# Performance work log

Measured on AMD Instinct MI355X. Metric: run time of the kernel, lower is better.

The kernel has to match this reference:

```python
import jax, jax.numpy as jnp
import numpy as np

N = 50000      # nodes
E = 600000     # message-passing edges (avg degree 12)
P = 500000     # candidate pairs
DH = 128       # d_h
NRBF = 16      # n_rbf
NL = 3         # n_layers
RBF_MAX = 1.5  # coords in [0,1]^2 -> max dist sqrt(2) ~ 1.414


def _mlp2(x, W1, b1, W2, b2):
    # mlp([a, b, c]) = Linear(a,b) -> ReLU -> Linear(b,c); dropout=0.0 is a no-op
    return jnp.dot(jax.nn.relu(jnp.dot(x, W1) + b1), W2) + b2


def _rbf(r):
    # Gaussian radial basis expansion of edge distances, NRBF centers on [0, RBF_MAX]
    centers = jnp.linspace(0.0, RBF_MAX, NRBF, dtype=r.dtype)
    width = centers[1] - centers[0]
    return jnp.exp(-jnp.square((r[:, None] - centers) / width))


def setup_inputs() -> dict:
    key = jax.random.key(0)
    ks = jax.random.split(key, 24)

    def lin(k, fan_in, fan_out):
        return jax.random.normal(k, (fan_in, fan_out), dtype=jnp.float32) / np.sqrt(fan_in)

    def lin_stack(k, n, fan_in, fan_out):
        return jax.random.normal(k, (n, fan_in, fan_out), dtype=jnp.float32) / np.sqrt(fan_in)

    inp = {}
    inp["coords01"] = jax.random.uniform(ks[0], (N, 2), dtype=jnp.float32)
    inp["msg_edge_index"] = jax.random.randint(ks[1], (2, E), 0, N)
    inp["cand_pairs_uv"] = jax.random.randint(ks[2], (P, 2), 0, N)
    # node_in: mlp([2, DH, DH])
    inp["node_W1"] = lin(ks[3], 2, DH)
    inp["node_b1"] = jnp.zeros((DH,), jnp.float32)
    inp["node_W2"] = lin(ks[4], DH, DH)
    inp["node_b2"] = jnp.zeros((DH,), jnp.float32)
    # per-layer InvariantMPNN params, stacked over NL layers
    # message MLP: [2*DH + NRBF, DH, DH]
    inp["msg_W1"] = lin_stack(ks[5], NL, 2 * DH + NRBF, DH)
    inp["msg_b1"] = jnp.zeros((NL, DH), jnp.float32)
    inp["msg_W2"] = lin_stack(ks[6], NL, DH, DH)
    inp["msg_b2"] = jnp.zeros((NL, DH), jnp.float32)
    # update MLP: [2*DH, DH, DH]
    inp["upd_W1"] = lin_stack(ks[7], NL, 2 * DH, DH)
    inp["upd_b1"] = jnp.zeros((NL, DH), jnp.float32)
    inp["upd_W2"] = lin_stack(ks[8], NL, DH, DH)
    inp["upd_b2"] = jnp.zeros((NL, DH), jnp.float32)
    # edge head: mlp([2*DH + 1, DH, 1])
    inp["head_W1"] = lin(ks[9], 2 * DH + 1, DH)
    inp["head_b1"] = jnp.zeros((DH,), jnp.float32)
    inp["head_W2"] = lin(ks[10], DH, 1)
    inp["head_b2"] = jnp.zeros((1,), jnp.float32)
    return inp


def reference(coords01, node_W1, node_b1, node_W2, node_b2,
              msg_W1, msg_b1, msg_W2, msg_b2,
              upd_W1, upd_b1, upd_W2, upd_b2,
              head_W1, head_b1, head_W2, head_b2,
              msg_edge_index, cand_pairs_uv):
    # node embedding from 2D coordinates
    h = _mlp2(coords01, node_W1, node_b1, node_W2, node_b2)  # [N, DH]

    src = msg_edge_index[0]
    dst = msg_edge_index[1]
    dx = coords01[src] - coords01[dst]                       # [E, 2]
    r = jnp.sqrt(jnp.sum(dx * dx, axis=-1) + 1e-8)           # [E]
    rbf = _rbf(r)                                            # [E, NRBF]

    # stacked invariant MPNN layers (residual)
    for l in range(NL):
        m_in = jnp.concatenate([h[src], h[dst], rbf], axis=-1)          # [E, 2*DH+NRBF]
        m = _mlp2(m_in, msg_W1[l], msg_b1[l], msg_W2[l], msg_b2[l])     # [E, DH]
        agg = jax.ops.segment_sum(m, dst, num_segments=N)               # [N, DH]
        u_in = jnp.concatenate([h, agg], axis=-1)                       # [N, 2*DH]
        h = h + _mlp2(u_in, upd_W1[l], upd_b1[l], upd_W2[l], upd_b2[l])

    # candidate edge scoring head
    u = cand_pairs_uv[:, 0]
    v = cand_pairs_uv[:, 1]
    dxc = coords01[u] - coords01[v]
    rc = jnp.sqrt(jnp.sum(dxc * dxc, axis=-1) + 1e-8)[:, None]          # [P, 1]
    edge_in = jnp.concatenate([h[u], h[v], rc], axis=-1)                # [P, 2*DH+1]
    logits = _mlp2(edge_in, head_W1, head_b1, head_W2, head_b2)[:, 0]   # [P]
    return logits
```

## Files before the change

kernel.cpp:

```cpp
#include <hip/hip_runtime.h>
#include <hip/hip_bf16.h>

#define NN 50000
#define NE 600000
#define NP 500000
#define DH 128
#define NRBF 16
#define NL 3

typedef __attribute__((ext_vector_type(8))) short bf16x8;
typedef __attribute__((ext_vector_type(4))) float f32x4;

__device__ __forceinline__ unsigned short f2b(float f){
  unsigned int u = __float_as_uint(f);
  u += 0x7fffu + ((u >> 16) & 1u);
  return (unsigned short)(u >> 16);
}
__device__ __forceinline__ float b2f(unsigned short u){
  return __uint_as_float(((unsigned)u) << 16);
}

__device__ __forceinline__ void zero_acc(f32x4 (&acc)[4][2]){
#pragma unroll
  for (int i=0;i<4;i++)
#pragma unroll
    for (int j=0;j<2;j++)
#pragma unroll
      for (int r=0;r<4;r++) acc[i][j][r]=0.f;
}

template<int RSB, int KB>
__device__ __forceinline__ void gemm_sw(const short* X, const short* __restrict__ Bp,
                                        int t, f32x4 (&acc)[4][2]){
  const int lane=t&63, w=t>>6, m=lane&15, g=lane>>4;
  const char* Xc = (const char*)X;
#pragma unroll
  for (int kb=0; kb<KB; kb++){
    bf16x8 a[4];
#pragma unroll
    for (int rt=0; rt<4; rt++){
      int ar = rt*16 + m;
      a[rt] = *reinterpret_cast<const bf16x8*>(Xc + ar*RSB + ((kb*64 + g*16) ^ ((ar&7)<<4)));
    }
#pragma unroll
    for (int c=0;c<2;c++){
      bf16x8 b = *reinterpret_cast<const bf16x8*>(Bp + ((size_t)((w*2+c)*KB+kb)*64 + lane)*8);
#pragma unroll
      for (int rt=0; rt<4; rt++)
        acc[rt][c] = __builtin_amdgcn_mfma_f32_16x16x32_bf16(a[rt], b, acc[rt][c], 0,0,0);
    }
  }
}

__global__ void pack_w_kernel(const float* __restrict__ W0, int Kr, int KB,
                              long wStride, long oStride, short* __restrict__ out0){
  int l = blockIdx.y;
  const float* W = W0 + (size_t)l*wStride;
  short* out = out0 + (size_t)l*oStride;
  int idx = blockIdx.x*256 + threadIdx.x;
  int total = 8*KB*64;
  if (idx >= total) return;
  int lane = idx & 63;
  int kb = (idx>>6) % KB;
  int ct = (idx>>6) / KB;
  int col = ct*16 + (lane&15);
  int k0 = kb*32 + 8*(lane>>4);
  bf16x8 pv;
#pragma unroll
  for (int e=0;e<8;e++){
    int k = k0+e;
    float f = (k<Kr) ? W[(size_t)k*DH + col] : 0.f;
    pv[e] = (short)f2b(f);
  }
  *reinterpret_cast<bf16x8*>(out + (size_t)idx*8) = pv;
}

__global__ void hist_kernel(const int* __restrict__ dstI, int* __restrict__ cnt){
  int e = blockIdx.x*256 + threadIdx.x;
  if (e < NE) atomicAdd(&cnt[dstI[e]], 1);
}

__global__ void scan_kernel(const int* __restrict__ cnt, int* __restrict__ rowptr){
  __shared__ int parts[1024];
  const int t = threadIdx.x;
  const int CH = (NN + 1023)/1024;
  int base = t*CH;
  int s = 0;
  for (int i=0;i<CH;i++){ int j=base+i; if (j<NN) s += cnt[j]; }
  parts[t] = s; __syncthreads();
  for (int off=1; off<1024; off<<=1){
    int v = (t>=off) ? parts[t-off] : 0;
    __syncthreads();
    parts[t] += v;
    __syncthreads();
  }
  int ex = (t==0) ? 0 : parts[t-1];
  for (int i=0;i<CH;i++){
    int j=base+i;
    if (j<NN){ rowptr[j] = ex; ex += cnt[j]; }
  }
  if (t==0) rowptr[NN] = NE;
}

__global__ void scatter_kernel(const int* __restrict__ srcI, const int* __restrict__ dstI,
                               int* __restrict__ ofs, int* __restrict__ ssrc,
                               int* __restrict__ sdst){
  int e = blockIdx.x*256 + threadIdx.x;
  if (e >= NE) return;
  int d = dstI[e];
  int p = atomicAdd(&ofs[d], 1);
  ssrc[p] = srcI[e];
  sdst[p] = d;
}

__global__ void rbf_kernel(const float* __restrict__ coords, const int* __restrict__ srcI,
                           const int* __restrict__ dstI, short* __restrict__ rbfp){
  int e = blockIdx.x*256 + threadIdx.x;
  if (e >= NE) return;
  int s = srcI[e], d = dstI[e];
  float dx = coords[2*s]-coords[2*d];
  float dy = coords[2*s+1]-coords[2*d+1];
  float r = sqrtf(dx*dx + dy*dy + 1e-8f);
  bf16x8 v0, v1;
#pragma unroll
  for (int i=0;i<8;i++){
    float t0 = (r - 0.1f*i)*10.f;
    v0[i] = (short)f2b(expf(-t0*t0));
    float t1 = (r - 0.1f*(i+8))*10.f;
    v1[i] = (short)f2b(expf(-t1*t1));
  }
  *reinterpret_cast<bf16x8*>(rbfp + (size_t)e*NRBF) = v0;
  *reinterpret_cast<bf16x8*>(rbfp + (size_t)e*NRBF + 8) = v1;
}

__global__ __launch_bounds__(256, 2) void node_kernel(
    const float* __restrict__ coords, const float* __restrict__ W1, const float* __restrict__ b1,
    const short* __restrict__ W2p, const float* __restrict__ b2,
    float* __restrict__ h, short* __restrict__ hbf)
{
  __shared__ __align__(16) short X[64*128];
  const int t = threadIdx.x;
  const int n0 = blockIdx.x*64;
  {
    int row = t >> 2;
    int n = n0 + row;
    float c0=0.f, c1=0.f;
    if (n < NN){ c0 = coords[2*n]; c1 = coords[2*n+1]; }
    char* Xc = (char*)X;
#pragma unroll
    for (int i=0;i<32;i++){
      int col = (t&3)*32 + i;
      float y = fmaxf(c0*W1[col] + c1*W1[DH+col] + b1[col], 0.f);
      *reinterpret_cast<short*>(Xc + row*256 + ((col*2) ^ ((row&7)<<4))) = (short)f2b(y);
    }
  }
  __syncthreads();
  f32x4 acc[4][2]; zero_acc(acc);
  gemm_sw<256,4>(X, W2p, t, acc);
  const int lane=t&63, w=t>>6, m=lane&15, g=lane>>4;
  float b2v0=b2[w*32+m], b2v1=b2[w*32+16+m];
#pragma unroll
  for (int rt=0;rt<4;rt++){
#pragma unroll
    for (int c=0;c<2;c++){
      float bb = c? b2v1 : b2v0;
      int col = (w*2+c)*16 + m;
#pragma unroll
      for (int r=0;r<4;r++){
        int row = rt*16 + g*4 + r;
        int n = n0 + row;
        if (n < NN){
          float val = acc[rt][c][r] + bb;
          h[(size_t)n*DH + col] = val;
          hbf[(size_t)n*DH + col] = (short)f2b(val);
        }
      }
    }
  }
}

__global__ __launch_bounds__(256, 2) void nodegemm2_f32(
    const short* __restrict__ hbf,
    const short* __restrict__ WpA, const float* __restrict__ biasA, float* __restrict__ outA,
    const short* __restrict__ WpB, float* __restrict__ outB)
{
  const int t=threadIdx.x, lane=t&63, w=t>>6, m=lane&15, g=lane>>4;
  const int n0 = blockIdx.x*64;
  f32x4 accA[4][2], accB[4][2]; zero_acc(accA); zero_acc(accB);
#pragma unroll
  for (int kb=0;kb<4;kb++){
    bf16x8 a[4];
#pragma unroll
    for (int rt=0;rt<4;rt++){
      int n = n0 + rt*16 + m; if (n >= NN) n = NN-1;
      a[rt] = *reinterpret_cast<const bf16x8*>(hbf + (size_t)n*DH + kb*32 + g*8);
    }
#pragma unroll
    for (int c=0;c<2;c++){
      bf16x8 bA = *reinterpret_cast<const bf16x8*>(WpA + ((size_t)((w*2+c)*4+kb)*64 + lane)*8);
      bf16x8 bB = *reinterpret_cast<const bf16x8*>(WpB + ((size_t)((w*2+c)*4+kb)*64 + lane)*8);
#pragma unroll
      for (int rt=0;rt<4;rt++){
        accA[rt][c] = __builtin_amdgcn_mfma_f32_16x16x32_bf16(a[rt], bA, accA[rt][c], 0,0,0);
        accB[rt][c] = __builtin_amdgcn_mfma_f32_16x16x32_bf16(a[rt], bB, accB[rt][c], 0,0,0);
      }
    }
  }
#pragma unroll
  for (int rt=0;rt<4;rt++){
#pragma unroll
    for (int c=0;c<2;c++){
      int col = (w*2+c)*16 + m;
      float bb = biasA ? biasA[col] : 0.f;
#pragma unroll
      for (int r=0;r<4;r++){
        int n = n0 + rt*16 + g*4 + r;
        if (n < NN){
          outA[(size_t)n*DH + col] = accA[rt][c][r] + bb;
          outB[(size_t)n*DH + col] = accB[rt][c][r];
        }
      }
    }
  }
}

__global__ __launch_bounds__(256, 3) void msg_kernel(
    const float* __restrict__ hA, const float* __restrict__ hB,
    const short* __restrict__ rbfp,
    const int* __restrict__ ssrc, const int* __restrict__ sdst,
    const short* __restrict__ W1cp, const short* __restrict__ W2p,
    const float* __restrict__ b2, float* __restrict__ agg)
{
  __shared__ __align__(16) short X[64*128];
  __shared__ float M[64][DH+1];
  __shared__ int srcl[64], dstl[64];
  const int t=threadIdx.x, lane=t&63, w=t>>6, m=lane&15, g=lane>>4;
  const int e0 = blockIdx.x*64;
  if (t < 64) srcl[t] = ssrc[e0+t];
  else if (t < 128) dstl[t-64] = sdst[e0+t-64];
  __syncthreads();

  f32x4 acc[4][2];
  {
    bf16x8 a[4];
#pragma unroll
    for (int rt=0;rt<4;rt++){
      if (g < 2)
        a[rt] = *reinterpret_cast<const bf16x8*>(rbfp + (size_t)(e0+rt*16+m)*NRBF + g*8);
      else {
        bf16x8 z;
#pragma unroll
        for (int e=0;e<8;e++) z[e]=0;
        a[rt]=z;
      }
    }
#pragma unroll
    for (int c=0;c<2;c++){
      bf16x8 b = *reinterpret_cast<const bf16x8*>(W1cp + ((size_t)(w*2+c)*64 + lane)*8);
      f32x4 z; z[0]=0.f; z[1]=0.f; z[2]=0.f; z[3]=0.f;
#pragma unroll
      for (int rt=0;rt<4;rt++)
        acc[rt][c] = __builtin_amdgcn_mfma_f32_16x16x32_bf16(a[rt], b, z, 0,0,0);
    }
  }
#pragma unroll
  for (int rt=0;rt<4;rt++){
#pragma unroll
    for (int r=0;r<4;r++){
      int row = rt*16 + g*4 + r;
      int s = srcl[row], d = dstl[row];
#pragma unroll
      for (int c=0;c<2;c++){
        int col = (w*2+c)*16 + m;
        acc[rt][c][r] += hA[(size_t)s*DH + col] + hB[(size_t)d*DH + col];
      }
    }
  }
  {
    char* Xc = (char*)X;
#pragma unroll
    for (int rt=0;rt<4;rt++){
#pragma unroll
      for (int c=0;c<2;c++){
        int col = (w*2+c)*16 + m;
#pragma unroll
        for (int r=0;r<4;r++){
          int row = rt*16 + g*4 + r;
          float y = fmaxf(acc[rt][c][r], 0.f);
          *reinterpret_cast<short*>(Xc + row*256 + ((col*2) ^ ((row&7)<<4))) = (short)f2b(y);
        }
      }
    }
  }
  __syncthreads();

  f32x4 acc2[4][2]; zero_acc(acc2);
  gemm_sw<256,4>(X, W2p, t, acc2);

  float b2v0=b2[w*32+m], b2v1=b2[w*32+16+m];
#pragma unroll
  for (int rt=0;rt<4;rt++){
#pragma unroll
    for (int c=0;c<2;c++){
      float bb = c? b2v1 : b2v0;
      int col = (w*2+c)*16 + m;
#pragma unroll
      for (int r=0;r<4;r++){
        int row = rt*16 + g*4 + r;
        M[row][col] = acc2[rt][c][r] + bb;
      }
    }
  }
  __syncthreads();

  {
    int col = t & 127, half = t >> 7;
    int r0 = half*32, r1 = r0 + 32;
    float s = 0.f;
    int cur = dstl[r0];
    for (int row=r0; row<r1; row++){
      int d = dstl[row];
      if (d != cur){
        atomicAdd(&agg[(size_t)cur*DH + col], s);
        s = 0.f; cur = d;
      }
      s += M[row][col];
    }
    atomicAdd(&agg[(size_t)cur*DH + col], s);
  }
}

__global__ __launch_bounds__(256, 2) void upd_kernel(
    const short* __restrict__ hbfin, const float* __restrict__ agg,
    const short* __restrict__ W1p, const float* __restrict__ b1,
    const short* __restrict__ W2p, const float* __restrict__ b2,
    float* __restrict__ h, short* __restrict__ hbfout)
{
  __shared__ __align__(16) short X[64*256];
  const int t = threadIdx.x;
  const int n0 = blockIdx.x*64;
  char* Xc = (char*)X;
#pragma unroll
  for (int j=0;j<4;j++){
    int slot = j*256 + t;
    int lane16 = slot & 15, row = slot >> 4;
    int n = n0 + row;
    int nc = n < NN ? n : NN-1;
    bf16x8 v = *reinterpret_cast<const bf16x8*>(hbfin + (size_t)nc*DH + lane16*8);
    *reinterpret_cast<bf16x8*>(Xc + row*512 + ((lane16*16) ^ ((row&7)<<4))) = v;
    const float* ap = agg + (size_t)nc*DH + lane16*8;
    bf16x8 o;
#pragma unroll
    for (int e=0;e<8;e++) o[e] = (short)f2b(ap[e]);
    *reinterpret_cast<bf16x8*>(Xc + row*512 + ((256 + lane16*16) ^ ((row&7)<<4))) = o;
  }
  __syncthreads();

  f32x4 acc[4][2]; zero_acc(acc);
  gemm_sw<512,8>(X, W1p, t, acc);
  __syncthreads();

  const int lane=t&63, w=t>>6, m=lane&15, g=lane>>4;
  float b1v0=b1[w*32+m], b1v1=b1[w*32+16+m];
#pragma unroll
  for (int rt=0;rt<4;rt++){
#pragma unroll
    for (int c=0;c<2;c++){
      float bb = c? b1v1 : b1v0;
      int col = (w*2+c)*16 + m;
#pragma unroll
      for (int r=0;r<4;r++){
        int row = rt*16 + g*4 + r;
        float y = fmaxf(acc[rt][c][r] + bb, 0.f);
        *reinterpret_cast<short*>(Xc + row*256 + ((col*2) ^ ((row&7)<<4))) = (short)f2b(y);
      }
    }
  }
  __syncthreads();

  f32x4 acc2[4][2]; zero_acc(acc2);
  gemm_sw<256,4>(X, W2p, t, acc2);

  float b2v0=b2[w*32+m], b2v1=b2[w*32+16+m];
#pragma unroll
  for (int rt=0;rt<4;rt++){
#pragma unroll
    for (int c=0;c<2;c++){
      float bb = c? b2v1 : b2v0;
      int col = (w*2+c)*16 + m;
#pragma unroll
      for (int r=0;r<4;r++){
        int row = rt*16 + g*4 + r;
        int n = n0 + row;
        if (n < NN){
          float val = h[(size_t)n*DH + col] + acc2[rt][c][r] + bb;
          h[(size_t)n*DH + col] = val;
          hbfout[(size_t)n*DH + col] = (short)f2b(val);
        }
      }
    }
  }
}

__global__ __launch_bounds__(256, 2) void head_kernel(
    const float* __restrict__ hU, const float* __restrict__ hV,
    const float* __restrict__ coords, const int* __restrict__ pairs,
    const float* __restrict__ w1r, const float* __restrict__ W2,
    const float* __restrict__ b2, float* __restrict__ out)
{
  const int t = threadIdx.x;
  const int l = t & 31;
  long p = (long)blockIdx.x*8 + (t>>5);
  int u = pairs[2*p], v = pairs[2*p+1];
  float dx = coords[2*u]-coords[2*v], dy = coords[2*u+1]-coords[2*v+1];
  float rc = sqrtf(dx*dx + dy*dy + 1e-8f);
  f32x4 a  = *reinterpret_cast<const f32x4*>(hU + (size_t)u*DH + l*4);
  f32x4 bb = *reinterpret_cast<const f32x4*>(hV + (size_t)v*DH + l*4);
  f32x4 wr = *reinterpret_cast<const f32x4*>(w1r + l*4);
  f32x4 w2 = *reinterpret_cast<const f32x4*>(W2 + l*4);
  float s = 0.f;
#pragma unroll
  for (int i=0;i<4;i++){
    float y = fmaxf(a[i] + bb[i] + rc*wr[i], 0.f);
    s += y * w2[i];
  }
#pragma unroll
  for (int off=1; off<32; off<<=1)
    s += __shfl_xor(s, off, 32);
  if (l == 0) out[p] = s + b2[0];
}

extern "C" void kernel_launch(void* const* d_in, const int* in_sizes, int n_in,
                              void* d_out, int out_size, void* d_ws, size_t ws_size,
                              hipStream_t stream)
{
  const float* coords  = (const float*)d_in[0];
  const int*   eidx    = (const int*)d_in[1];
  const int*   pairs   = (const int*)d_in[2];
  const float* node_W1 = (const float*)d_in[3];
  const float* node_b1 = (const float*)d_in[4];
  const float* node_W2 = (const float*)d_in[5];
  const float* node_b2 = (const float*)d_in[6];
  const float* msg_W1  = (const float*)d_in[7];
  const float* msg_b1  = (const float*)d_in[8];
  const float* msg_W2  = (const float*)d_in[9];
  const float* msg_b2  = (const float*)d_in[10];
  const float* upd_W1  = (const float*)d_in[11];
  const float* upd_b1  = (const float*)d_in[12];
  const float* upd_W2  = (const float*)d_in[13];
  const float* upd_b2  = (const float*)d_in[14];
  const float* head_W1 = (const float*)d_in[15];
  const float* head_b1 = (const float*)d_in[16];
  const float* head_W2 = (const float*)d_in[17];
  const float* head_b2 = (const float*)d_in[18];

  char* ws = (char*)d_ws;
  size_t off = 0;
  auto alloc = [&](size_t bytes)->void*{ void* p = ws + off; off += (bytes + 255) & ~(size_t)255; return p; };
  float* h      = (float*)alloc((size_t)NN*DH*4);
  short* hbf    = (short*)alloc((size_t)NN*DH*2);
  short* rbfp   = (short*)alloc((size_t)NE*NRBF*2);
  float* hA     = (float*)alloc((size_t)NN*DH*4);
  float* hB     = (float*)alloc((size_t)NN*DH*4);
  float* agg    = (float*)alloc((size_t)NN*DH*4);
  int*   ssrc   = (int*)alloc((size_t)NE*4);
  int*   sdst   = (int*)alloc((size_t)NE*4);
  int*   cnt    = (int*)alloc((size_t)NN*4);
  int*   rowptr = (int*)alloc((size_t)(NN+1)*4);
  int*   ofs    = (int*)alloc((size_t)NN*4);
  short* msgW1ap= (short*)alloc((size_t)NL*4*4096*2);
  short* msgW1bp= (short*)alloc((size_t)NL*4*4096*2);
  short* msgW1cp= (short*)alloc((size_t)NL*1*4096*2);
  short* msgW2p = (short*)alloc((size_t)NL*4*4096*2);
  short* updW1p = (short*)alloc((size_t)NL*8*4096*2);
  short* updW2p = (short*)alloc((size_t)NL*4*4096*2);
  short* headUp = (short*)alloc((size_t)4*4096*2);
  short* headVp = (short*)alloc((size_t)4*4096*2);
  short* nodeW2p= (short*)alloc((size_t)4*4096*2);

  const int* srcI = eidx;
  const int* dstI = eidx + NE;

  hipMemsetAsync(cnt, 0, (size_t)NN*4, stream);
  hist_kernel<<<(NE+255)/256, 256, 0, stream>>>(dstI, cnt);
  scan_kernel<<<1, 1024, 0, stream>>>(cnt, rowptr);
  hipMemcpyAsync(ofs, rowptr, (size_t)NN*4, hipMemcpyDeviceToDevice, stream);
  scatter_kernel<<<(NE+255)/256, 256, 0, stream>>>(srcI, dstI, ofs, ssrc, sdst);

  rbf_kernel<<<(NE+255)/256, 256, 0, stream>>>(coords, ssrc, sdst, rbfp);

  {
    dim3 g4((8*4*64+255)/256, NL), g1((8*1*64+255)/256, NL), g8((8*8*64+255)/256, NL);
    pack_w_kernel<<<g4, 256, 0, stream>>>(msg_W1,          128, 4, (long)272*DH, 4*4096, msgW1ap);
    pack_w_kernel<<<g4, 256, 0, stream>>>(msg_W1 + 128*DH, 128, 4, (long)272*DH, 4*4096, msgW1bp);
    pack_w_kernel<<<g1, 256, 0, stream>>>(msg_W1 + 256*DH,  16, 1, (long)272*DH, 1*4096, msgW1cp);
    pack_w_kernel<<<g4, 256, 0, stream>>>(msg_W2, 128, 4, (long)DH*DH, 4*4096, msgW2p);
    pack_w_kernel<<<g8, 256, 0, stream>>>(upd_W1, 256, 8, (long)256*DH, 8*4096, updW1p);
    pack_w_kernel<<<g4, 256, 0, stream>>>(upd_W2, 128, 4, (long)DH*DH, 4*4096, updW2p);
    dim3 s4((8*4*64+255)/256, 1);
    pack_w_kernel<<<s4, 256, 0, stream>>>(head_W1,          128, 4, 0, 0, headUp);
    pack_w_kernel<<<s4, 256, 0, stream>>>(head_W1 + 128*DH, 128, 4, 0, 0, headVp);
    pack_w_kernel<<<s4, 256, 0, stream>>>(node_W2, 128, 4, 0, 0, nodeW2p);
  }

  node_kernel<<<(NN+63)/64, 256, 0, stream>>>(coords, node_W1, node_b1, nodeW2p, node_b2, h, hbf);

  const int NB = (NN+63)/64;
  for (int l=0; l<NL; l++){
    nodegemm2_f32<<<NB, 256, 0, stream>>>(hbf,
        msgW1ap + (size_t)l*4*4096, msg_b1 + l*DH, hA,
        msgW1bp + (size_t)l*4*4096, hB);
    hipMemsetAsync(agg, 0, (size_t)NN*DH*4, stream);
    msg_kernel<<<NE/64, 256, 0, stream>>>(hA, hB, rbfp, ssrc, sdst,
        msgW1cp + (size_t)l*1*4096, msgW2p + (size_t)l*4*4096, msg_b2 + l*DH, agg);
    upd_kernel<<<NB, 256, 0, stream>>>(hbf, agg,
        updW1p + (size_t)l*8*4096, upd_b1 + l*DH,
        updW2p + (size_t)l*4*4096, upd_b2 + l*DH, h, hbf);
  }

  nodegemm2_f32<<<NB, 256, 0, stream>>>(hbf, headUp, head_b1, hA, headVp, hB);
  head_kernel<<<NP/8, 256, 0, stream>>>(hA, hB, coords, pairs,
      head_W1 + 256*DH, head_W2, head_b2, (float*)d_out);
}
```

Before: 835.7 us.

## Sort candidate pairs by source node and reuse LDS tile for message reduction

Adds a counting sort of candidate pairs by u (histogram, scan, scatter) so the head kernel reads hU rows with locality, and writes outputs back through a permutation index. In msg_kernel, the fp32 M staging buffer is dropped and the bf16 swizzled X tile is reused for the second-layer output, cutting LDS use so the launch-bounds occupancy hint rises from 3 to 6 blocks per SM. This trades extra sort kernels and bf16 rounding of messages before aggregation for less LDS pressure and better cache reuse in the head. Scratch buffers ssrc, sdst and rbfp are reused for the sorted pairs after the message-passing layers.

```diff
diff --git a/kernel.cpp b/kernel.cpp
--- a/kernel.cpp
+++ b/kernel.cpp
@@ -75,12 +75,13 @@
   *reinterpret_cast<bf16x8*>(out + (size_t)idx*8) = pv;
 }
 
-__global__ void hist_kernel(const int* __restrict__ dstI, int* __restrict__ cnt){
+__global__ void hist_kernel(const int* __restrict__ keys, int stride, int n,
+                            int* __restrict__ cnt){
   int e = blockIdx.x*256 + threadIdx.x;
-  if (e < NE) atomicAdd(&cnt[dstI[e]], 1);
-}
-
-__global__ void scan_kernel(const int* __restrict__ cnt, int* __restrict__ rowptr){
+  if (e < n) atomicAdd(&cnt[keys[(size_t)e*stride]], 1);
+}
+
+__global__ void scan_kernel(const int* __restrict__ cnt, int total, int* __restrict__ rowptr){
   __shared__ int parts[1024];
   const int t = threadIdx.x;
   const int CH = (NN + 1023)/1024;
@@ -99,7 +100,7 @@
     int j=base+i;
     if (j<NN){ rowptr[j] = ex; ex += cnt[j]; }
   }
-  if (t==0) rowptr[NN] = NE;
+  if (t==0) rowptr[NN] = total;
 }
 
 __global__ void scatter_kernel(const int* __restrict__ srcI, const int* __restrict__ dstI,
@@ -111,6 +112,16 @@
   int p = atomicAdd(&ofs[d], 1);
   ssrc[p] = srcI[e];
   sdst[p] = d;
+}
+
+__global__ void pair_scatter_kernel(const int* __restrict__ pairs, int* __restrict__ ofs,
+                                    int* __restrict__ su, int* __restrict__ sv,
+                                    int* __restrict__ sidx){
+  int p = blockIdx.x*256 + threadIdx.x;
+  if (p >= NP) return;
+  int u = pairs[2*p], v = pairs[2*p+1];
+  int pos = atomicAdd(&ofs[u], 1);
+  su[pos] = u; sv[pos] = v; sidx[pos] = p;
 }
 
 __global__ void rbf_kernel(const float* __restrict__ coords, const int* __restrict__ srcI,
@@ -224,7 +235,7 @@
   }
 }
 
-__global__ __launch_bounds__(256, 3) void msg_kernel(
+__global__ __launch_bounds__(256, 6) void msg_kernel(
     const float* __restrict__ hA, const float* __restrict__ hB,
     const short* __restrict__ rbfp,
     const int* __restrict__ ssrc, const int* __restrict__ sdst,
@@ -232,7 +243,6 @@
     const float* __restrict__ b2, float* __restrict__ agg)
 {
   __shared__ __align__(16) short X[64*128];
-  __shared__ float M[64][DH+1];
   __shared__ int srcl[64], dstl[64];
   const int t=threadIdx.x, lane=t&63, w=t>>6, m=lane&15, g=lane>>4;
   const int e0 = blockIdx.x*64;
@@ -296,24 +306,30 @@
 
   f32x4 acc2[4][2]; zero_acc(acc2);
   gemm_sw<256,4>(X, W2p, t, acc2);
+  __syncthreads();
 
   float b2v0=b2[w*32+m], b2v1=b2[w*32+16+m];
-#pragma unroll
-  for (int rt=0;rt<4;rt++){
-#pragma unroll
-    for (int c=0;c<2;c++){
-      float bb = c? b2v1 : b2v0;
-      int col = (w*2+c)*16 + m;
-#pragma unroll
-      for (int r=0;r<4;r++){
-        int row = rt*16 + g*4 + r;
-        M[row][col] = acc2[rt][c][r] + bb;
-      }
-    }
-  }
-  __syncthreads();
-
   {
+    char* Xc = (char*)X;
+#pragma unroll
+    for (int rt=0;rt<4;rt++){
+#pragma unroll
+      for (int c=0;c<2;c++){
+        float bb = c? b2v1 : b2v0;
+        int col = (w*2+c)*16 + m;
+#pragma unroll
+        for (int r=0;r<4;r++){
+          int row = rt*16 + g*4 + r;
+          *reinterpret_cast<short*>(Xc + row*256 + ((col*2) ^ ((row&7)<<4))) =
+              (short)f2b(acc2[rt][c][r] + bb);
+        }
+      }
+    }
+  }
+  __syncthreads();
+
+  {
+    const char* Xc = (const char*)X;
     int col = t & 127, half = t >> 7;
     int r0 = half*32, r1 = r0 + 32;
     float s = 0.f;
@@ -324,7 +340,8 @@
         atomicAdd(&agg[(size_t)cur*DH + col], s);
         s = 0.f; cur = d;
       }
-      s += M[row][col];
+      s += b2f(*reinterpret_cast<const unsigned short*>(
+               Xc + row*256 + ((col*2) ^ ((row&7)<<4))));
     }
     atomicAdd(&agg[(size_t)cur*DH + col], s);
   }
@@ -404,14 +421,16 @@
 
 __global__ __launch_bounds__(256, 2) void head_kernel(
     const float* __restrict__ hU, const float* __restrict__ hV,
-    const float* __restrict__ coords, const int* __restrict__ pairs,
+    const float* __restrict__ coords,
+    const int* __restrict__ su, const int* __restrict__ sv,
+    const int* __restrict__ sidx,
     const float* __restrict__ w1r, const float* __restrict__ W2,
     const float* __restrict__ b2, float* __restrict__ out)
 {
   const int t = threadIdx.x;
   const int l = t & 31;
   long p = (long)blockIdx.x*8 + (t>>5);
-  int u = pairs[2*p], v = pairs[2*p+1];
+  int u = su[p], v = sv[p];
   float dx = coords[2*u]-coords[2*v], dy = coords[2*u+1]-coords[2*v+1];
   float rc = sqrtf(dx*dx + dy*dy + 1e-8f);
   f32x4 a  = *reinterpret_cast<const f32x4*>(hU + (size_t)u*DH + l*4);
@@ -427,7 +446,7 @@
 #pragma unroll
   for (int off=1; off<32; off<<=1)
     s += __shfl_xor(s, off, 32);
-  if (l == 0) out[p] = s + b2[0];
+  if (l == 0) out[sidx[p]] = s + b2[0];
 }
 
 extern "C" void kernel_launch(void* const* d_in, const int* in_sizes, int n_in,
@@ -482,8 +501,8 @@
   const int* dstI = eidx + NE;
 
   hipMemsetAsync(cnt, 0, (size_t)NN*4, stream);
-  hist_kernel<<<(NE+255)/256, 256, 0, stream>>>(dstI, cnt);
-  scan_kernel<<<1, 1024, 0, stream>>>(cnt, rowptr);
+  hist_kernel<<<(NE+255)/256, 256, 0, stream>>>(dstI, 1, NE, cnt);
+  scan_kernel<<<1, 1024, 0, stream>>>(cnt, NE, rowptr);
   hipMemcpyAsync(ofs, rowptr, (size_t)NN*4, hipMemcpyDeviceToDevice, stream);
   scatter_kernel<<<(NE+255)/256, 256, 0, stream>>>(srcI, dstI, ofs, ssrc, sdst);
 
@@ -518,7 +537,16 @@
         updW2p + (size_t)l*4*4096, upd_b2 + l*DH, h, hbf);
   }
 
+  int* su   = ssrc;
+  int* sv   = sdst;
+  int* sidx = (int*)rbfp;
+  hipMemsetAsync(cnt, 0, (size_t)NN*4, stream);
+  hist_kernel<<<(NP+255)/256, 256, 0, stream>>>(pairs, 2, NP, cnt);
+  scan_kernel<<<1, 1024, 0, stream>>>(cnt, NP, rowptr);
+  hipMemcpyAsync(ofs, rowptr, (size_t)NN*4, hipMemcpyDeviceToDevice, stream);
+  pair_scatter_kernel<<<(NP+255)/256, 256, 0, stream>>>(pairs, ofs, su, sv, sidx);
+
   nodegemm2_f32<<<NB, 256, 0, stream>>>(hbf, headUp, head_b1, hA, headVp, hB);
-  head_kernel<<<NP/8, 256, 0, stream>>>(hA, hB, coords, pairs,
+  head_kernel<<<NP/8, 256, 0, stream>>>(hA, hB, coords, su, sv, sidx,
       head_W1 + 256*DH, head_W2, head_b2, (float*)d_out);
 }
```

Measured after the change: 1.123 ms. +34.4%, slower.
